# Optimization experiments

Hardware: AMD Instinct MI355X
Metric: run time of the kernel (lower is better)

The kernel has to match this reference:

```python
import jax, jax.numpy as jnp
import numpy as np

IN_SIZE, OUT_SIZE, EDGE_SIZE = 32, 32, 16
NET_LAYERS = [128, 128]          # cfg.net_layers (hidden sizes of the edge MLP)
B, N_NEIGH = 10000, 20           # nodes x neighbors
E = B * N_NEIGH                  # total edges


def setup_inputs() -> dict:
    key = jax.random.key(0)
    ks = jax.random.split(key, 16)
    h_v = jax.random.normal(ks[0], (B, N_NEIGH), jnp.float32)
    h_w = jax.random.normal(ks[1], (B, IN_SIZE), jnp.float32)
    e_vw = jax.random.normal(ks[2], (E, EDGE_SIZE), jnp.float32)
    dims = [EDGE_SIZE] + NET_LAYERS + [IN_SIZE * OUT_SIZE]
    params = {}
    for i, (din, dout) in enumerate(zip(dims[:-1], dims[1:])):
        bound = 1.0 / np.sqrt(din)  # torch nn.Linear default init
        params[f"W{i}"] = jax.random.uniform(ks[3 + 2 * i], (dout, din), jnp.float32, -bound, bound)
        params[f"b{i}"] = jax.random.uniform(ks[4 + 2 * i], (dout,), jnp.float32, -bound, bound)
    return {"h_v": h_v, "h_w": h_w, "e_vw": e_vw, **params}


def reference(h_v, h_w, e_vw, W0, b0, W1, b1, W2, b2):
    # Edge MLP: edge_size -> 128 -> 128 -> in*out (ReLU on hidden layers only)
    x = jax.nn.relu(e_vw @ W0.T + b0)
    x = jax.nn.relu(x @ W1.T + b1)
    m = (x @ W2.T + b2).reshape(-1, OUT_SIZE, IN_SIZE)  # [E, out, in]

    # Faithful reproduction of h_w[..., None].expand(B, in, n).view(-1, in)
    n = h_v.shape[1]
    h_w_rows = jnp.broadcast_to(h_w[:, :, None], (h_w.shape[0], IN_SIZE, n)).reshape(-1, IN_SIZE)  # [E, in]

    # bmm(m, h_w_rows[..., None]).squeeze() -> [E, out]
    out = jnp.einsum("eoi,ei->eo", m, h_w_rows)
    return jnp.squeeze(out)
```

## Files before the change

### kernel.cpp

```cpp
#include <hip/hip_runtime.h>


typedef __bf16 bf16x8 __attribute__((ext_vector_type(8)));
typedef float  f32x4  __attribute__((ext_vector_type(4)));

#define NB       10000
#define NNEIGH   20
#define PADH     136
#define NBT      157
#define EPAD     10048

#define WS_W0S   0
#define WS_W1S   8192
#define WS_W2GS  40960
#define WS_B2G   532480
#define WS_HWG   540160
#define WS_X1    2940160

__device__ __forceinline__ unsigned short f2bf(float f) {
    unsigned int u = __float_as_uint(f);
    unsigned int r = (u + 0x7fffu + ((u >> 16) & 1u)) >> 16;
    return (unsigned short)r;
}
__device__ __forceinline__ unsigned int pack2(float a, float b) {
    return (unsigned int)f2bf(a) | ((unsigned int)f2bf(b) << 16);
}

__global__ __launch_bounds__(256) void prep_kernel(
    const float* __restrict__ W0, const float* __restrict__ b0,
    const float* __restrict__ W1,
    const float* __restrict__ W2, const float* __restrict__ b2,
    const float* __restrict__ h_w,
    unsigned short* __restrict__ w0s, unsigned short* __restrict__ w1s,
    unsigned short* __restrict__ w2gs, float* __restrict__ b2g,
    float* __restrict__ hwg)
{
    const int bx = blockIdx.x, tid = threadIdx.x;
    if (bx < 16) {
        int gid = bx * 256 + tid;
        int o = gid >> 7, k = gid & 127;
        const int ka = k >> 5, quad = (k >> 3) & 3, j = k & 7;
        float pref[32];
        float run = 0.f;
#pragma unroll
        for (int i = 0; i < 32; ++i) {
            run += W2[(size_t)(32 * o + i) * 128 + k];
            pref[i] = run;
        }
#pragma unroll
        for (int kn = 0; kn < 20; ++kn) {
            const int j0 = (32 * kn) / 20;
#pragma unroll
            for (int g = 0; g < 3; ++g) {
                int lo = 20 * (j0 + g) - 32 * kn;     if (lo < 0) lo = 0;
                int hi = 20 * (j0 + g + 1) - 32 * kn; if (hi > 32) hi = 32;
                float v = (hi > lo) ? (pref[hi - 1] - (lo > 0 ? pref[lo - 1] : 0.f)) : 0.f;
                int c = g * 32 + o;
                int ct = c >> 4, lq = c & 15;
                int lane = quad * 16 + lq;
                w2gs[(size_t)(((kn * 6 + ct) * 4 + ka) * 64 + lane) * 8 + j] = f2bf(v);
            }
        }
    } else if (bx == 16) {
        for (int t = 0; t < 16; ++t) {
            int idx = t * 256 + tid;
            int ct = idx >> 9, lane = (idx >> 3) & 63, j = idx & 7;
            int lq = lane & 15, q = lane >> 4;
            int k = q * 8 + j, o = ct * 16 + lq;
            float v = (k < 16) ? W0[o * 16 + k] : (k == 16 ? b0[o] : 0.f);
            w0s[idx] = f2bf(v);
        }
    } else if (bx <= 32) {
        for (int t = 0; t < 4; ++t) {
            int idx = (bx - 17) * 1024 + t * 256 + tid;
            int ct = idx >> 11, ka = (idx >> 9) & 3, lane = (idx >> 3) & 63, j = idx & 7;
            int lq = lane & 15, q = lane >> 4;
            w1s[idx] = f2bf(W1[(ct * 16 + lq) * 128 + ka * 32 + q * 8 + j]);
        }
    } else if (bx == 33) {
        for (int idx = tid; idx < 1920; idx += 256) {
            int kn = idx / 96, rem = idx - kn * 96;
            int g = rem >> 5, o = rem & 31;
            int j0 = (32 * kn) / 20;
            int lo = 20 * (j0 + g) - 32 * kn;     if (lo < 0) lo = 0;
            int hi = 20 * (j0 + g + 1) - 32 * kn; if (hi > 32) hi = 32;
            float s = 0.f;
            for (int i = lo; i < hi; ++i) s += b2[32 * o + i];
            b2g[idx] = s;
        }
    } else {
#pragma unroll
        for (int t = 0; t < 4; ++t) {
            int idx = (bx - 34) * 1024 + t * 256 + tid;
            if (idx < 600000) {
                int kn3 = idx / 10000, b = idx - kn3 * 10000;
                int kn = kn3 / 3, g = kn3 - kn * 3;
                int jv = (32 * kn) / 20 + g; if (jv > 31) jv = 31;
                hwg[idx] = h_w[b * 32 + jv];
            }
        }
    }
}

__global__ __launch_bounds__(256) void k1_kernel(
    const float* __restrict__ e_vw, const float* __restrict__ b1v,
    const unsigned short* __restrict__ w0s, const unsigned short* __restrict__ w1s,
    unsigned short* __restrict__ x1)
{
    __shared__ __align__(16) unsigned short sX[64 * PADH];

    const int tid = threadIdx.x;
    const int lane = tid & 63, w = tid >> 6;
    const int quad = lane >> 4, lq = lane & 15;
    const int kn = blockIdx.y;
    const int rbase = w * 16;
    const int e = blockIdx.x * 64 + rbase + lq;
    const unsigned short one_bf = 0x3f80;

    const unsigned short* w0base = w0s + lane * 8;
    const unsigned short* w1base = w1s + lane * 8;

    union { bf16x8 v; uint4 u; } B;
    B.u = make_uint4(0u, 0u, 0u, 0u);
    if (quad < 2) {
        if (e < NB) {
            const float4* p = (const float4*)(e_vw + ((size_t)e * NNEIGH + kn) * 16 + quad * 8);
            float4 f0 = p[0], f1 = p[1];
            B.u = make_uint4(pack2(f0.x, f0.y), pack2(f0.z, f0.w),
                             pack2(f1.x, f1.y), pack2(f1.z, f1.w));
        }
    } else if (quad == 2) {
        B.u.x = (unsigned int)one_bf;
    }

#pragma unroll
    for (int ct = 0; ct < 8; ++ct) {
        bf16x8 wf = *(const bf16x8*)(w0base + ct * 512);
        f32x4 acc = {0.f, 0.f, 0.f, 0.f};
        acc = __builtin_amdgcn_mfma_f32_16x16x32_bf16(wf, B.v, acc, 0, 0, 0);
#pragma unroll
        for (int r2 = 0; r2 < 4; ++r2) acc[r2] = acc[r2] > 0.f ? acc[r2] : 0.f;
        uint2 pk = make_uint2(pack2(acc[0], acc[1]), pack2(acc[2], acc[3]));
        *(uint2*)&sX[(rbase + lq) * PADH + ct * 16 + quad * 4] = pk;
    }

    {
        bf16x8 xf[4];
#pragma unroll
        for (int ka = 0; ka < 4; ++ka)
            xf[ka] = *(const bf16x8*)&sX[(rbase + lq) * PADH + ka * 32 + quad * 8];
        unsigned short* xout = x1 + ((size_t)kn * EPAD + e) * 128;
#pragma unroll
        for (int ct = 0; ct < 8; ++ct) {
            f32x4 acc = *(const f32x4*)(b1v + ct * 16 + quad * 4);
#pragma unroll
            for (int ka = 0; ka < 4; ++ka) {
                bf16x8 wf = *(const bf16x8*)(w1base + (ct * 4 + ka) * 512);
                acc = __builtin_amdgcn_mfma_f32_16x16x32_bf16(wf, xf[ka], acc, 0, 0, 0);
            }
#pragma unroll
            for (int r2 = 0; r2 < 4; ++r2) acc[r2] = acc[r2] > 0.f ? acc[r2] : 0.f;
            *(uint2*)(xout + ct * 16 + quad * 4) =
                make_uint2(pack2(acc[0], acc[1]), pack2(acc[2], acc[3]));
        }
    }
}

__global__ __launch_bounds__(256) void k2_kernel(
    const float* __restrict__ hwg, const unsigned short* __restrict__ x1,
    const unsigned short* __restrict__ w2gs, const float* __restrict__ b2g,
    float* __restrict__ out)
{
    const int tid = threadIdx.x;
    const int lane = tid & 63, w = tid >> 6;
    const int quad = lane >> 4, lq = lane & 15;
    const int kn = blockIdx.y;
    const int e = blockIdx.x * 64 + w * 16 + lq;
    const bool three = ((32 * kn) % 20) > 8;

    const unsigned short* w2base = w2gs + (size_t)kn * 6 * 4 * 512 + lane * 8;

    bf16x8 xf[4];
    const unsigned short* xin = x1 + ((size_t)kn * EPAD + e) * 128;
#pragma unroll
    for (int ka = 0; ka < 4; ++ka)
        xf[ka] = *(const bf16x8*)(xin + ka * 32 + quad * 8);

    float hw0 = (e < NB) ? hwg[(kn * 3 + 0) * NB + e] : 0.f;
    float hw1 = (e < NB) ? hwg[(kn * 3 + 1) * NB + e] : 0.f;
    float hw2 = (three && e < NB) ? hwg[(kn * 3 + 2) * NB + e] : 0.f;

    f32x4 accC[6];
#pragma unroll
    for (int ct = 0; ct < 4; ++ct) {
        const unsigned short* wp = w2base + (size_t)ct * 4 * 512;
        f32x4 acc = *(const f32x4*)(b2g + kn * 96 + ct * 16 + quad * 4);
#pragma unroll
        for (int ka = 0; ka < 4; ++ka) {
            bf16x8 wf = *(const bf16x8*)(wp + ka * 512);
            acc = __builtin_amdgcn_mfma_f32_16x16x32_bf16(wf, xf[ka], acc, 0, 0, 0);
        }
        accC[ct] = acc;
    }
    if (three) {
#pragma unroll
        for (int ct = 4; ct < 6; ++ct) {
            const unsigned short* wp = w2base + (size_t)ct * 4 * 512;
            f32x4 acc = *(const f32x4*)(b2g + kn * 96 + ct * 16 + quad * 4);
#pragma unroll
            for (int ka = 0; ka < 4; ++ka) {
                bf16x8 wf = *(const bf16x8*)(wp + ka * 512);
                acc = __builtin_amdgcn_mfma_f32_16x16x32_bf16(wf, xf[ka], acc, 0, 0, 0);
            }
            accC[ct] = acc;
        }
    }
    if (e < NB) {
#pragma unroll
        for (int half = 0; half < 2; ++half) {
            float4 val;
            float* vp = &val.x;
#pragma unroll
            for (int r2 = 0; r2 < 4; ++r2) {
                float s = hw0 * accC[half][r2] + hw1 * accC[2 + half][r2];
                if (three) s += hw2 * accC[4 + half][r2];
                vp[r2] = s;
            }
            *(float4*)(out + ((size_t)e * NNEIGH + kn) * 32 + half * 16 + quad * 4) = val;
        }
    }
}

extern "C" void kernel_launch(void* const* d_in, const int* in_sizes, int n_in,
                              void* d_out, int out_size, void* d_ws, size_t ws_size,
                              hipStream_t stream)
{
    const float* h_w = (const float*)d_in[1];
    const float* e_vw = (const float*)d_in[2];
    const float* W0 = (const float*)d_in[3];
    const float* b0 = (const float*)d_in[4];
    const float* W1 = (const float*)d_in[5];
    const float* b1 = (const float*)d_in[6];
    const float* W2 = (const float*)d_in[7];
    const float* b2 = (const float*)d_in[8];
    float* out = (float*)d_out;

    char* ws = (char*)d_ws;
    unsigned short* w0s  = (unsigned short*)(ws + WS_W0S);
    unsigned short* w1s  = (unsigned short*)(ws + WS_W1S);
    unsigned short* w2gs = (unsigned short*)(ws + WS_W2GS);
    float*          b2g  = (float*)(ws + WS_B2G);
    float*          hwg  = (float*)(ws + WS_HWG);
    unsigned short* x1   = (unsigned short*)(ws + WS_X1);

    prep_kernel<<<620, 256, 0, stream>>>(W0, b0, W1, W2, b2, h_w,
                                         w0s, w1s, w2gs, b2g, hwg);
    dim3 grid(NBT, 20);
    k1_kernel<<<grid, 256, 0, stream>>>(e_vw, b1, w0s, w1s, x1);
    k2_kernel<<<grid, 256, 0, stream>>>(hwg, x1, w2gs, b2g, out);
}
```

Measured before the change: 154.0 us.

## Make MLP kernels persistent over edge tiles with weights kept in LDS and registers

Both kernels now launch 39 blocks per neighbor instead of 157 and each block loops over several 64-edge tiles. k1 stages W1 into shared memory and keeps W0 fragments in registers, and it prefetches the next tile's edge features. k2 keeps W2 fragments and the bias in registers across tiles. The goal is to stop reloading weights from global memory for every tile. In exchange the grid is smaller (780 blocks), which may leave CUs idle, and the extra registers and the 32KB of LDS reduce occupancy.

```diff
diff --git a/kernel.cpp b/kernel.cpp
--- a/kernel.cpp
+++ b/kernel.cpp
@@ -7,6 +7,7 @@
 #define NB       10000
 #define NNEIGH   20
 #define PADH     136
+#define NCHUNK   39
 #define NBT      157
 #define EPAD     10048
 
@@ -107,61 +108,88 @@
     const unsigned short* __restrict__ w0s, const unsigned short* __restrict__ w1s,
     unsigned short* __restrict__ x1)
 {
+    __shared__ __align__(16) unsigned short sW1f[16384];
     __shared__ __align__(16) unsigned short sX[64 * PADH];
 
     const int tid = threadIdx.x;
     const int lane = tid & 63, w = tid >> 6;
     const int quad = lane >> 4, lq = lane & 15;
-    const int kn = blockIdx.y;
+    const int kn = blockIdx.y, chunk = blockIdx.x;
     const int rbase = w * 16;
-    const int e = blockIdx.x * 64 + rbase + lq;
     const unsigned short one_bf = 0x3f80;
 
-    const unsigned short* w0base = w0s + lane * 8;
-    const unsigned short* w1base = w1s + lane * 8;
-
-    union { bf16x8 v; uint4 u; } B;
-    B.u = make_uint4(0u, 0u, 0u, 0u);
-    if (quad < 2) {
-        if (e < NB) {
+    {
+        const uint4* src = (const uint4*)w1s;
+        uint4* dst = (uint4*)sW1f;
+        for (int i = tid; i < 2048; i += 256) dst[i] = src[i];
+    }
+    bf16x8 w0f[8];
+#pragma unroll
+    for (int ct = 0; ct < 8; ++ct)
+        w0f[ct] = *(const bf16x8*)(w0s + (ct * 64 + lane) * 8);
+    __syncthreads();
+
+    const unsigned short* sW1base = sW1f + lane * 8;
+
+    float4 f0, f1;
+    {
+        const int e = chunk * 64 + rbase + lq;
+        if (quad < 2 && e < NB) {
             const float4* p = (const float4*)(e_vw + ((size_t)e * NNEIGH + kn) * 16 + quad * 8);
-            float4 f0 = p[0], f1 = p[1];
-            B.u = make_uint4(pack2(f0.x, f0.y), pack2(f0.z, f0.w),
-                             pack2(f1.x, f1.y), pack2(f1.z, f1.w));
-        }
-    } else if (quad == 2) {
-        B.u.x = (unsigned int)one_bf;
-    }
-
-#pragma unroll
-    for (int ct = 0; ct < 8; ++ct) {
-        bf16x8 wf = *(const bf16x8*)(w0base + ct * 512);
-        f32x4 acc = {0.f, 0.f, 0.f, 0.f};
-        acc = __builtin_amdgcn_mfma_f32_16x16x32_bf16(wf, B.v, acc, 0, 0, 0);
-#pragma unroll
-        for (int r2 = 0; r2 < 4; ++r2) acc[r2] = acc[r2] > 0.f ? acc[r2] : 0.f;
-        uint2 pk = make_uint2(pack2(acc[0], acc[1]), pack2(acc[2], acc[3]));
-        *(uint2*)&sX[(rbase + lq) * PADH + ct * 16 + quad * 4] = pk;
-    }
-
-    {
-        bf16x8 xf[4];
-#pragma unroll
-        for (int ka = 0; ka < 4; ++ka)
-            xf[ka] = *(const bf16x8*)&sX[(rbase + lq) * PADH + ka * 32 + quad * 8];
-        unsigned short* xout = x1 + ((size_t)kn * EPAD + e) * 128;
+            f0 = p[0]; f1 = p[1];
+        }
+    }
+
+    for (int btile = chunk; btile < NBT; btile += NCHUNK) {
+        const int e = btile * 64 + rbase + lq;
+
+        union { bf16x8 v; uint4 u; } B;
+        B.u = make_uint4(0u, 0u, 0u, 0u);
+        if (quad < 2) {
+            if (e < NB)
+                B.u = make_uint4(pack2(f0.x, f0.y), pack2(f0.z, f0.w),
+                                 pack2(f1.x, f1.y), pack2(f1.z, f1.w));
+        } else if (quad == 2) {
+            B.u.x = (unsigned int)one_bf;
+        }
+
+        {
+            const int ne = (btile + NCHUNK) * 64 + rbase + lq;
+            if (btile + NCHUNK < NBT && quad < 2 && ne < NB) {
+                const float4* p = (const float4*)(e_vw + ((size_t)ne * NNEIGH + kn) * 16 + quad * 8);
+                f0 = p[0]; f1 = p[1];
+            }
+        }
+
 #pragma unroll
         for (int ct = 0; ct < 8; ++ct) {
-            f32x4 acc = *(const f32x4*)(b1v + ct * 16 + quad * 4);
-#pragma unroll
-            for (int ka = 0; ka < 4; ++ka) {
-                bf16x8 wf = *(const bf16x8*)(w1base + (ct * 4 + ka) * 512);
-                acc = __builtin_amdgcn_mfma_f32_16x16x32_bf16(wf, xf[ka], acc, 0, 0, 0);
-            }
+            f32x4 acc = {0.f, 0.f, 0.f, 0.f};
+            acc = __builtin_amdgcn_mfma_f32_16x16x32_bf16(w0f[ct], B.v, acc, 0, 0, 0);
 #pragma unroll
             for (int r2 = 0; r2 < 4; ++r2) acc[r2] = acc[r2] > 0.f ? acc[r2] : 0.f;
-            *(uint2*)(xout + ct * 16 + quad * 4) =
-                make_uint2(pack2(acc[0], acc[1]), pack2(acc[2], acc[3]));
+            uint2 pk = make_uint2(pack2(acc[0], acc[1]), pack2(acc[2], acc[3]));
+            *(uint2*)&sX[(rbase + lq) * PADH + ct * 16 + quad * 4] = pk;
+        }
+
+        {
+            bf16x8 xf[4];
+#pragma unroll
+            for (int ka = 0; ka < 4; ++ka)
+                xf[ka] = *(const bf16x8*)&sX[(rbase + lq) * PADH + ka * 32 + quad * 8];
+            unsigned short* xout = x1 + ((size_t)kn * EPAD + e) * 128;
+#pragma unroll
+            for (int ct = 0; ct < 8; ++ct) {
+                f32x4 acc = *(const f32x4*)(b1v + ct * 16 + quad * 4);
+#pragma unroll
+                for (int ka = 0; ka < 4; ++ka) {
+                    bf16x8 wf = *(const bf16x8*)(sW1base + (ct * 4 + ka) * 512);
+                    acc = __builtin_amdgcn_mfma_f32_16x16x32_bf16(wf, xf[ka], acc, 0, 0, 0);
+                }
+#pragma unroll
+                for (int r2 = 0; r2 < 4; ++r2) acc[r2] = acc[r2] > 0.f ? acc[r2] : 0.f;
+                *(uint2*)(xout + ct * 16 + quad * 4) =
+                    make_uint2(pack2(acc[0], acc[1]), pack2(acc[2], acc[3]));
+            }
         }
     }
 }
@@ -174,59 +202,74 @@
     const int tid = threadIdx.x;
     const int lane = tid & 63, w = tid >> 6;
     const int quad = lane >> 4, lq = lane & 15;
-    const int kn = blockIdx.y;
-    const int e = blockIdx.x * 64 + w * 16 + lq;
+    const int kn = blockIdx.y, chunk = blockIdx.x;
+    const int rbase = w * 16;
     const bool three = ((32 * kn) % 20) > 8;
 
     const unsigned short* w2base = w2gs + (size_t)kn * 6 * 4 * 512 + lane * 8;
-
-    bf16x8 xf[4];
-    const unsigned short* xin = x1 + ((size_t)kn * EPAD + e) * 128;
-#pragma unroll
-    for (int ka = 0; ka < 4; ++ka)
-        xf[ka] = *(const bf16x8*)(xin + ka * 32 + quad * 8);
-
-    float hw0 = (e < NB) ? hwg[(kn * 3 + 0) * NB + e] : 0.f;
-    float hw1 = (e < NB) ? hwg[(kn * 3 + 1) * NB + e] : 0.f;
-    float hw2 = (three && e < NB) ? hwg[(kn * 3 + 2) * NB + e] : 0.f;
-
-    f32x4 accC[6];
-#pragma unroll
-    for (int ct = 0; ct < 4; ++ct) {
-        const unsigned short* wp = w2base + (size_t)ct * 4 * 512;
-        f32x4 acc = *(const f32x4*)(b2g + kn * 96 + ct * 16 + quad * 4);
-#pragma unroll
-        for (int ka = 0; ka < 4; ++ka) {
-            bf16x8 wf = *(const bf16x8*)(wp + ka * 512);
-            acc = __builtin_amdgcn_mfma_f32_16x16x32_bf16(wf, xf[ka], acc, 0, 0, 0);
-        }
-        accC[ct] = acc;
-    }
+    bf16x8 w2f[6][4];
+#pragma unroll
+    for (int ct = 0; ct < 4; ++ct)
+#pragma unroll
+        for (int ka = 0; ka < 4; ++ka)
+            w2f[ct][ka] = *(const bf16x8*)(w2base + (size_t)(ct * 4 + ka) * 512);
     if (three) {
 #pragma unroll
-        for (int ct = 4; ct < 6; ++ct) {
-            const unsigned short* wp = w2base + (size_t)ct * 4 * 512;
-            f32x4 acc = *(const f32x4*)(b2g + kn * 96 + ct * 16 + quad * 4);
-#pragma unroll
-            for (int ka = 0; ka < 4; ++ka) {
-                bf16x8 wf = *(const bf16x8*)(wp + ka * 512);
-                acc = __builtin_amdgcn_mfma_f32_16x16x32_bf16(wf, xf[ka], acc, 0, 0, 0);
-            }
+        for (int ct = 4; ct < 6; ++ct)
+#pragma unroll
+            for (int ka = 0; ka < 4; ++ka)
+                w2f[ct][ka] = *(const bf16x8*)(w2base + (size_t)(ct * 4 + ka) * 512);
+    }
+    f32x4 b2r[6];
+#pragma unroll
+    for (int ct = 0; ct < 6; ++ct)
+        b2r[ct] = *(const f32x4*)(b2g + kn * 96 + ct * 16 + quad * 4);
+
+    for (int btile = chunk; btile < NBT; btile += NCHUNK) {
+        const int e = btile * 64 + rbase + lq;
+
+        bf16x8 xf[4];
+        const unsigned short* xin = x1 + ((size_t)kn * EPAD + e) * 128;
+#pragma unroll
+        for (int ka = 0; ka < 4; ++ka)
+            xf[ka] = *(const bf16x8*)(xin + ka * 32 + quad * 8);
+
+        float hw0 = (e < NB) ? hwg[(kn * 3 + 0) * NB + e] : 0.f;
+        float hw1 = (e < NB) ? hwg[(kn * 3 + 1) * NB + e] : 0.f;
+        float hw2 = (three && e < NB) ? hwg[(kn * 3 + 2) * NB + e] : 0.f;
+
+        f32x4 accC[6];
+#pragma unroll
+        for (int ct = 0; ct < 4; ++ct) {
+            f32x4 acc = b2r[ct];
+#pragma unroll
+            for (int ka = 0; ka < 4; ++ka)
+                acc = __builtin_amdgcn_mfma_f32_16x16x32_bf16(w2f[ct][ka], xf[ka], acc, 0, 0, 0);
             accC[ct] = acc;
         }
-    }
-    if (e < NB) {
-#pragma unroll
-        for (int half = 0; half < 2; ++half) {
-            float4 val;
-            float* vp = &val.x;
-#pragma unroll
-            for (int r2 = 0; r2 < 4; ++r2) {
-                float s = hw0 * accC[half][r2] + hw1 * accC[2 + half][r2];
-                if (three) s += hw2 * accC[4 + half][r2];
-                vp[r2] = s;
-            }
-            *(float4*)(out + ((size_t)e * NNEIGH + kn) * 32 + half * 16 + quad * 4) = val;
+        if (three) {
+#pragma unroll
+            for (int ct = 4; ct < 6; ++ct) {
+                f32x4 acc = b2r[ct];
+#pragma unroll
+                for (int ka = 0; ka < 4; ++ka)
+                    acc = __builtin_amdgcn_mfma_f32_16x16x32_bf16(w2f[ct][ka], xf[ka], acc, 0, 0, 0);
+                accC[ct] = acc;
+            }
+        }
+        if (e < NB) {
+#pragma unroll
+            for (int half = 0; half < 2; ++half) {
+                float4 val;
+                float* vp = &val.x;
+#pragma unroll
+                for (int r2 = 0; r2 < 4; ++r2) {
+                    float s = hw0 * accC[half][r2] + hw1 * accC[2 + half][r2];
+                    if (three) s += hw2 * accC[4 + half][r2];
+                    vp[r2] = s;
+                }
+                *(float4*)(out + ((size_t)e * NNEIGH + kn) * 32 + half * 16 + quad * 4) = val;
+            }
         }
     }
 }
@@ -255,7 +298,7 @@
 
     prep_kernel<<<620, 256, 0, stream>>>(W0, b0, W1, W2, b2, h_w,
                                          w0s, w1s, w2gs, b2g, hwg);
-    dim3 grid(NBT, 20);
+    dim3 grid(NCHUNK, 20);
     k1_kernel<<<grid, 256, 0, stream>>>(e_vw, b1, w0s, w1s, x1);
     k2_kernel<<<grid, 256, 0, stream>>>(hwg, x1, w2gs, b2g, out);
 }
```

Result: faster. 139.2 us (-9.6%).
